# Kernel tuning notes

Measured on AMD Instinct MI355X. Metric: run time of the kernel, lower is better.

## Reference

```python
import jax, jax.numpy as jnp
import numpy as np

N_NODES = 50000
N_EDGES = 1600000
IN_CH = 512
HID_CH = 256


def _gcn_conv(x, edge_index, W, b):
    """PyG-style GCNConv: add self-loops, symmetric normalization, x@W then aggregate."""
    n = x.shape[0]
    loop = jnp.arange(n, dtype=edge_index.dtype)
    src = jnp.concatenate([edge_index[0], loop])  # [E+N]
    dst = jnp.concatenate([edge_index[1], loop])  # [E+N]
    deg = jax.ops.segment_sum(jnp.ones_like(dst, dtype=x.dtype), dst, num_segments=n)
    dinv = jnp.where(deg > 0, jax.lax.rsqrt(deg), 0.0)
    norm = dinv[src] * dinv[dst]  # [E+N]
    h = x @ W  # transform first (smaller feature dim for aggregation)
    msg = h[src] * norm[:, None]  # [E+N, F_out]
    out = jax.ops.segment_sum(msg, dst, num_segments=n)
    return out + b


def setup_inputs() -> dict:
    key = jax.random.key(0)
    ks = jax.random.split(key, 8)
    x = jax.random.normal(ks[0], (N_NODES, IN_CH), dtype=jnp.float32)
    edge_index = jax.random.randint(ks[1], (2, N_EDGES), 0, N_NODES, dtype=jnp.int32)
    W1 = jax.random.normal(ks[2], (IN_CH, HID_CH), dtype=jnp.float32) * (1.0 / np.sqrt(IN_CH))
    b1 = jnp.zeros((HID_CH,), dtype=jnp.float32)
    W2 = jax.random.normal(ks[3], (HID_CH, 32), dtype=jnp.float32) * (1.0 / np.sqrt(HID_CH))
    b2 = jnp.zeros((32,), dtype=jnp.float32)
    Wl = jax.random.normal(ks[4], (32, 2), dtype=jnp.float32) * (1.0 / np.sqrt(32))
    bl = jnp.zeros((2,), dtype=jnp.float32)
    return {"x": x, "edge_index": edge_index, "W1": W1, "b1": b1,
            "W2": W2, "b2": b2, "Wl": Wl, "bl": bl}


def reference(x, edge_index, W1, b1, W2, b2, Wl, bl):
    h = _gcn_conv(x, edge_index, W1, b1)
    h = jax.nn.relu(h)
    h = _gcn_conv(h, edge_index, W2, b2)
    # F.dropout(training=...) treated as identity (eval-mode reference)
    logits = h @ Wl + bl
    return jax.nn.log_softmax(logits, axis=1)
```

## Files before the change

### kernel.cpp

```cpp
#include <hip/hip_runtime.h>
#include <hip/hip_bf16.h>
#include <stdint.h>

#define NN 50000
#define NE 1600000
#define CIN 512
#define CH1 256
#define CH2 32

#define NBUCK 196
#define CAP 10240
#define CAP2 16384
#define ECH 4096
#define NCH 391

typedef __bf16 bf16_t;
typedef __attribute__((ext_vector_type(2))) __bf16 bf16x2;
typedef __attribute__((ext_vector_type(8))) __bf16 bf16x8;
typedef __attribute__((ext_vector_type(4))) float f32x4;

__device__ inline float blo(uint32_t v) { return __uint_as_float(v << 16); }
__device__ inline float bhi(uint32_t v) { return __uint_as_float(v & 0xffff0000u); }
__device__ inline uint32_t pk2(float a, float b) {
  bf16x2 p; p[0] = (__bf16)a; p[1] = (__bf16)b; return *(uint32_t*)&p;
}

__global__ __launch_bounds__(256) void k_hist(const int* __restrict__ dst,
                                              int* __restrict__ counts) {
  __shared__ int h[256];
  int blk = blockIdx.x, t = threadIdx.x;
  int e0 = blk * ECH;
  int ce = NE - e0; if (ce > ECH) ce = ECH;
  h[t] = 0;
  __syncthreads();
  for (int k = t; k < ce; k += 256) atomicAdd(&h[dst[e0 + k] >> 8], 1);
  __syncthreads();
  if (t < NBUCK) counts[blk * NBUCK + t] = h[t];
}

__global__ __launch_bounds__(512) void k_scanb(const int* __restrict__ counts,
                                               int* __restrict__ offs,
                                               int* __restrict__ bcnt) {
  __shared__ int l[512];
  int b = blockIdx.x, t = threadIdx.x;
  int v = (t < NCH) ? counts[t * NBUCK + b] : 0;
  int x = v;
  l[t] = x;
  __syncthreads();
  for (int off = 1; off < 512; off <<= 1) {
    int u = (t >= off) ? l[t - off] : 0;
    __syncthreads();
    x += u; l[t] = x;
    __syncthreads();
  }
  if (t < NCH) offs[t * NBUCK + b] = b * CAP + (x - v);
  if (t == 511) bcnt[b] = x;
}

__global__ __launch_bounds__(256) void k_bin(const int* __restrict__ src,
    const int* __restrict__ dst, const int* __restrict__ offs,
    uint32_t* __restrict__ binned) {
  __shared__ int h[256], lbase[256], lcnt[256], offsL[256];
  __shared__ uint32_t lstage[ECH];
  int blk = blockIdx.x, t = threadIdx.x;
  int e0 = blk * ECH;
  int ce = NE - e0; if (ce > ECH) ce = ECH;
  h[t] = 0; lcnt[t] = 0;
  if (t < NBUCK) offsL[t] = offs[blk * NBUCK + t];
  __syncthreads();
  for (int k = t; k < ce; k += 256) atomicAdd(&h[dst[e0 + k] >> 8], 1);
  __syncthreads();
  int v = h[t], x = v;
  lbase[t] = x;
  __syncthreads();
  for (int off = 1; off < 256; off <<= 1) {
    int u = (t >= off) ? lbase[t - off] : 0;
    __syncthreads();
    x += u; lbase[t] = x;
    __syncthreads();
  }
  lbase[t] = x - v;
  __syncthreads();
  for (int k = t; k < ce; k += 256) {
    int d = dst[e0 + k], s = src[e0 + k];
    int bkt = d >> 8;
    int p = lbase[bkt] + atomicAdd(&lcnt[bkt], 1);
    lstage[p] = ((uint32_t)bkt << 24) | ((uint32_t)(d & 255) << 16) | (uint32_t)s;
  }
  __syncthreads();
  for (int j = t; j < ce; j += 256) {
    uint32_t e = lstage[j];
    int bkt = e >> 24;
    binned[offsL[bkt] + (j - lbase[bkt])] = e & 0x00ffffffu;
  }
}

__global__ __launch_bounds__(256) void k_build(const uint32_t* __restrict__ binned,
    const int* __restrict__ bcnt, int* __restrict__ rowptr2, int* __restrict__ deg2,
    float* __restrict__ dinv, uint16_t* __restrict__ csrs) {
  __shared__ int hist[256], prow[256], lcnt[256];
  __shared__ int tot_s;
  __shared__ uint32_t c2[CAP2];
  int b = blockIdx.x, t = threadIdx.x;
  int count = bcnt[b];
  hist[t] = 0; lcnt[t] = 0;
  __syncthreads();
  const uint32_t* bb = binned + (size_t)b * CAP;
  for (int j = t; j < count; j += 256) atomicAdd(&hist[bb[j] >> 16], 1);
  __syncthreads();
  int node = b * 256 + t;
  int deg = hist[t];
  int pdeg = (node < NN) ? ((deg + 16) & ~15) : 0;
  int x = pdeg;
  prow[t] = x;
  __syncthreads();
  for (int off = 1; off < 256; off <<= 1) {
    int u = (t >= off) ? prow[t - off] : 0;
    __syncthreads();
    x += u; prow[t] = x;
    __syncthreads();
  }
  int start = x - pdeg;
  prow[t] = start;
  if (t == 255) tot_s = x;
  if (node < NN) {
    rowptr2[node] = b * CAP2 + start;
    deg2[node] = pdeg;
    dinv[node] = 1.0f / sqrtf((float)(deg + 1));
    c2[start + deg] = (uint32_t)node;
    for (int k = deg + 1; k < pdeg; ++k)
      c2[start + k] = (uint32_t)NN;
  }
  __syncthreads();
  for (int j = t; j < count; j += 256) {
    uint32_t e = bb[j];
    int dl = e >> 16;
    int p = prow[dl] + atomicAdd(&lcnt[dl], 1);
    c2[p] = e & 0xffffu;
  }
  __syncthreads();
  int tot = tot_s;
  uint16_t* co = csrs + (size_t)b * CAP2;
  for (int j = t; j < tot; j += 256) co[j] = (uint16_t)c2[j];
}

__global__ void k_prep_w(const float* __restrict__ W1, const float* __restrict__ W2,
                         bf16_t* __restrict__ w1t, bf16_t* __restrict__ w2t,
                         uint32_t* __restrict__ h1p_u32, uint32_t* __restrict__ h2b_u32) {
  int i = blockIdx.x * 256 + threadIdx.x;
  if (i < CIN * CH1) {
    int n = i >> 9, k = i & 511;
    w1t[i] = (__bf16)W1[k * CH1 + n];
  }
  if (i < CH1 * CH2) {
    int oc = i >> 8, k = i & 255;
    w2t[i] = (__bf16)W2[k * CH2 + oc];
  }
  if (blockIdx.x == 0) {
    int t = threadIdx.x;
    if (t < 128) {
      int p = t >> 4;
      h1p_u32[((size_t)p * (NN + 1) + NN) * 16 + (t & 15)] = 0;
    } else if (t < 144) {
      h2b_u32[(size_t)NN * 16 + (t - 128)] = 0;
    }
  }
}

#define BM 128
#define BN 128
#define BK 64

__global__ __launch_bounds__(256) void k_gemm1(const float* __restrict__ X,
                                               const bf16_t* __restrict__ BT,
                                               const float* __restrict__ dinv,
                                               bf16_t* __restrict__ h1p) {
  __shared__ __align__(16) bf16_t ldsA[2][BM * BK];
  __shared__ __align__(16) bf16_t ldsB[2][BN * BK];
  const int tid = threadIdx.x;
  const int lane = tid & 63;
  const int wid = tid >> 6;
  const int tm = blockIdx.x, tn = blockIdx.y;
  const int wm = wid >> 1, wn = wid & 1;

  f32x4 acc[4][4] = {};
  float4 ra[4], rb[4];

  auto loadA = [&](int kt) {
#pragma unroll
    for (int q = 0; q < 4; ++q) {
      int idx16 = q * 256 + tid;
      int r = idx16 >> 3, cw = idx16 & 7;
      int grow = tm * BM + r;
      grow = grow < NN ? grow : NN - 1;
      const float* ga = X + (size_t)grow * CIN + kt * BK + cw * 8;
      ra[q] = *(const float4*)ga;
      rb[q] = *(const float4*)(ga + 4);
    }
  };
  auto writeA = [&](int buf) {
#pragma unroll
    for (int q = 0; q < 4; ++q) {
      int idx16 = q * 256 + tid;
      int r = idx16 >> 3, cw = idx16 & 7;
      bf16x8 o;
      o[0] = (__bf16)ra[q].x; o[1] = (__bf16)ra[q].y;
      o[2] = (__bf16)ra[q].z; o[3] = (__bf16)ra[q].w;
      o[4] = (__bf16)rb[q].x; o[5] = (__bf16)rb[q].y;
      o[6] = (__bf16)rb[q].z; o[7] = (__bf16)rb[q].w;
      *(bf16x8*)&ldsA[buf][r * 64 + ((cw ^ (r & 7)) << 3)] = o;
    }
  };
  auto stageB = [&](int buf, int kt) {
#pragma unroll
    for (int t = 0; t < 4; ++t) {
      int o = t * 4096 + tid * 16;
      int r = o >> 7, cw = (o >> 4) & 7;
      int lc = cw ^ (r & 7);
      const bf16_t* gb = BT + (size_t)(tn * BN + r) * CIN + kt * BK + lc * 8;
      __builtin_amdgcn_global_load_lds(
          (const __attribute__((address_space(1))) void*)gb,
          (__attribute__((address_space(3))) void*)&ldsB[buf][(t * 4096 + wid * 1024) >> 1],
          16, 0, 0);
    }
  };

  loadA(0);
  stageB(0, 0);
  writeA(0);
  __syncthreads();
  int cur = 0;
  for (int kt = 0; kt < CIN / BK; ++kt) {
    if (kt + 1 < CIN / BK) { loadA(kt + 1); stageB(cur ^ 1, kt + 1); }
#pragma unroll
    for (int ks = 0; ks < 2; ++ks) {
      bf16x8 af[4], bfr[4];
#pragma unroll
      for (int m = 0; m < 4; ++m) {
        int row = wm * 64 + m * 16 + (lane & 15);
        int kc = ks * 4 + (lane >> 4);
        af[m] = *(const bf16x8*)&ldsA[cur][row * 64 + ((kc ^ (row & 7)) << 3)];
      }
#pragma unroll
      for (int n = 0; n < 4; ++n) {
        int col = wn * 64 + n * 16 + (lane & 15);
        int kc = ks * 4 + (lane >> 4);
        bfr[n] = *(const bf16x8*)&ldsB[cur][col * 64 + ((kc ^ (col & 7)) << 3)];
      }
#pragma unroll
      for (int m = 0; m < 4; ++m)
#pragma unroll
        for (int n = 0; n < 4; ++n)
          acc[m][n] = __builtin_amdgcn_mfma_f32_16x16x32_bf16(af[m], bfr[n], acc[m][n], 0, 0, 0);
    }
    if (kt + 1 < CIN / BK) writeA(cur ^ 1);
    __syncthreads();
    cur ^= 1;
  }

#pragma unroll
  for (int m = 0; m < 4; ++m) {
#pragma unroll
    for (int r = 0; r < 4; ++r) {
      int grow = tm * BM + wm * 64 + m * 16 + (lane >> 4) * 4 + r;
      if (grow < NN) {
        float dv = dinv[grow];
#pragma unroll
        for (int n = 0; n < 4; ++n) {
          int gcol = tn * BN + wn * 64 + n * 16 + (lane & 15);
          int plane = gcol >> 5, pc = gcol & 31;
          h1p[(size_t)plane * ((NN + 1) * 32) + (size_t)grow * 32 + pc] =
              (__bf16)(dv * acc[m][n][r]);
        }
      }
    }
  }
}

__global__ __launch_bounds__(256) void k_agg1(const uint32_t* __restrict__ h1p,
    const int* __restrict__ rowptr2, const int* __restrict__ deg2,
    const uint16_t* __restrict__ csrs, const float* __restrict__ dinv,
    const float* __restrict__ bias, uint32_t* __restrict__ hrp) {
  const int s = blockIdx.x & 7;
  const int lane = threadIdx.x & 63;
  const int wid = threadIdx.x >> 6;
  const int i = (blockIdx.x >> 3) * 16 + wid * 4 + (lane >> 4);
  const int cl = lane & 15;
  const uint32_t* __restrict__ P = h1p + (size_t)s * ((NN + 1) * 16);

  float a0 = 0.f, a1 = 0.f;
  const int base = rowptr2[i];
  const int pdeg = deg2[i];
  for (int b0 = 0; b0 < pdeg; b0 += 16) {
    int ld = (int)__builtin_nontemporal_load(&csrs[base + b0 + cl]);
#pragma unroll
    for (int e = 0; e < 16; ++e) {
      int src = __shfl(ld, (lane & 48) + e);
      uint32_t v = P[(src << 4) + cl];
      a0 += blo(v); a1 += bhi(v);
    }
  }
  float di = dinv[i];
  float2 bb = *(const float2*)&bias[s * 32 + cl * 2];
  uint32_t o = pk2(fmaxf(di * a0 + bb.x, 0.f), fmaxf(di * a1 + bb.y, 0.f));
  __builtin_nontemporal_store(o, &hrp[((size_t)s * NN + i) * 16 + cl]);
}

__global__ __launch_bounds__(256) void k_gemm2(const bf16_t* __restrict__ hrp,
    const bf16_t* __restrict__ w2t, const float* __restrict__ dinv,
    bf16_t* __restrict__ h2b) {
  const int lane = threadIdx.x & 63;
  const int gw = blockIdx.x * 4 + (threadIdx.x >> 6);
  const int r0 = gw * 16;
  if (r0 >= NN) return;
  int arow = r0 + (lane & 15);
  arow = arow < NN ? arow : NN - 1;
  const int kc = lane >> 4;
  f32x4 acc0 = {}, acc1 = {};
#pragma unroll
  for (int kb = 0; kb < 8; ++kb) {
    bf16x8 a  = *(const bf16x8*)&hrp[(size_t)kb * (NN * 32) + (size_t)arow * 32 + kc * 8];
    bf16x8 b0 = *(const bf16x8*)&w2t[(size_t)(lane & 15) * CH1 + kb * 32 + kc * 8];
    bf16x8 b1 = *(const bf16x8*)&w2t[(size_t)(16 + (lane & 15)) * CH1 + kb * 32 + kc * 8];
    acc0 = __builtin_amdgcn_mfma_f32_16x16x32_bf16(a, b0, acc0, 0, 0, 0);
    acc1 = __builtin_amdgcn_mfma_f32_16x16x32_bf16(a, b1, acc1, 0, 0, 0);
  }
#pragma unroll
  for (int r = 0; r < 4; ++r) {
    int rr = r0 + (lane >> 4) * 4 + r;
    if (rr < NN) {
      float dv = dinv[rr];
      h2b[(size_t)rr * CH2 + (lane & 15)]      = (__bf16)(dv * acc0[r]);
      h2b[(size_t)rr * CH2 + 16 + (lane & 15)] = (__bf16)(dv * acc1[r]);
    }
  }
}

__global__ __launch_bounds__(256) void k_agg2(const uint32_t* __restrict__ h2b,
    const int* __restrict__ rowptr2, const int* __restrict__ deg2,
    const uint16_t* __restrict__ csrs, const float* __restrict__ dinv,
    const float* __restrict__ b2, const float* __restrict__ Wl,
    const float* __restrict__ bl, float* __restrict__ out) {
  const int lane = threadIdx.x & 63;
  const int wid = threadIdx.x >> 6;
  const int i = blockIdx.x * 16 + wid * 4 + (lane >> 4);
  const int cl = lane & 15;

  float a0 = 0.f, a1 = 0.f;
  const int base = rowptr2[i];
  const int pdeg = deg2[i];
  for (int b0 = 0; b0 < pdeg; b0 += 16) {
    int ld = (int)__builtin_nontemporal_load(&csrs[base + b0 + cl]);
#pragma unroll
    for (int e = 0; e < 16; ++e) {
      int src = __shfl(ld, (lane & 48) + e);
      uint32_t v = h2b[(src << 4) + cl];
      a0 += blo(v); a1 += bhi(v);
    }
  }
  float di = dinv[i];
  float vv0 = di * a0 + b2[cl * 2];
  float vv1 = di * a1 + b2[cl * 2 + 1];
  const float2* Wl2 = (const float2*)Wl;
  float2 w0 = Wl2[cl * 2], w1 = Wl2[cl * 2 + 1];
  float lp0 = vv0 * w0.x + vv1 * w1.x;
  float lp1 = vv0 * w0.y + vv1 * w1.y;
#pragma unroll
  for (int off = 1; off < 16; off <<= 1) {
    lp0 += __shfl_xor(lp0, off);
    lp1 += __shfl_xor(lp1, off);
  }
  if (cl == 0) {
    float l0 = lp0 + bl[0], l1 = lp1 + bl[1];
    float m = fmaxf(l0, l1);
    float lse = m + logf(expf(l0 - m) + expf(l1 - m));
    float2 o; o.x = l0 - lse; o.y = l1 - lse;
    *(float2*)&out[i * 2] = o;
  }
}

extern "C" void kernel_launch(void* const* d_in, const int* in_sizes, int n_in,
                              void* d_out, int out_size, void* d_ws, size_t ws_size,
                              hipStream_t stream) {
  const float* x  = (const float*)d_in[0];
  const int*   ei = (const int*)d_in[1];
  const float* W1 = (const float*)d_in[2];
  const float* b1 = (const float*)d_in[3];
  const float* W2 = (const float*)d_in[4];
  const float* b2 = (const float*)d_in[5];
  const float* Wl = (const float*)d_in[6];
  const float* bl = (const float*)d_in[7];
  float* out = (float*)d_out;

  const int* src = ei;
  const int* dst = ei + NE;

  uint8_t* w = (uint8_t*)d_ws;
  auto alloc = [&](size_t bytes) { void* p = w; w += (bytes + 255) & ~(size_t)255; return p; };
  int*      counts = (int*)alloc((size_t)NCH * NBUCK * 4);
  int*      offs   = (int*)alloc((size_t)NCH * NBUCK * 4);
  int*      bcnt   = (int*)alloc((size_t)NBUCK * 4);
  uint32_t* binned = (uint32_t*)alloc((size_t)NBUCK * CAP * 4);
  uint16_t* csrs   = (uint16_t*)alloc((size_t)NBUCK * CAP2 * 2);
  int*      rowptr2= (int*)alloc((size_t)NN * 4);
  int*      deg2   = (int*)alloc((size_t)NN * 4);
  float*    dinv   = (float*)alloc((size_t)NN * 4);
  bf16_t*   w1t    = (bf16_t*)alloc((size_t)CIN * CH1 * 2);
  bf16_t*   w2t    = (bf16_t*)alloc((size_t)CH1 * CH2 * 2);
  bf16_t*   h1p    = (bf16_t*)alloc((size_t)(NN + 1) * CH1 * 2);
  bf16_t*   hrp    = (bf16_t*)alloc((size_t)NN * CH1 * 2);
  bf16_t*   h2b    = (bf16_t*)alloc((size_t)(NN + 1) * CH2 * 2);

  k_hist <<<NCH, 256, 0, stream>>>(dst, counts);
  k_scanb<<<NBUCK, 512, 0, stream>>>(counts, offs, bcnt);
  k_bin  <<<NCH, 256, 0, stream>>>(src, dst, offs, binned);
  k_build<<<NBUCK, 256, 0, stream>>>(binned, bcnt, rowptr2, deg2, dinv, csrs);

  k_prep_w<<<(CIN * CH1 + 255) / 256, 256, 0, stream>>>(W1, W2, w1t, w2t,
                                                        (uint32_t*)h1p, (uint32_t*)h2b);

  dim3 g1((NN + BM - 1) / BM, CH1 / BN);
  k_gemm1<<<g1, 256, 0, stream>>>(x, w1t, dinv, h1p);

  k_agg1<<<(NN / 16) * 8, 256, 0, stream>>>((const uint32_t*)h1p, rowptr2, deg2,
                                            csrs, dinv, b1, (uint32_t*)hrp);
  k_gemm2<<<(NN / 16 + 3) / 4, 256, 0, stream>>>(hrp, w2t, dinv, h2b);
  k_agg2<<<NN / 16, 256, 0, stream>>>((const uint32_t*)h2b, rowptr2, deg2, csrs,
                                      dinv, b2, Wl, bl, out);
}
```

Measured before the change: 231.9 us.

## Use 4 lanes per node with 16-byte gathers in aggregation kernels

Both aggregation kernels now map 4 lanes per destination node instead of 16. Each lane gathers 16 bytes (8 bf16 channels) per neighbour through a vectorized load, and neighbour indices are read as packed uint32 pairs and prefetched one chunk ahead. This cuts the number of memory instructions and shuffles per edge and raises the number of nodes per wave, which helps hide load latency. The cost is more registers per lane and a padded-degree assumption of multiples of 8, where reads past the end of a row rely on the padding layout.

```diff
diff --git a/kernel.cpp b/kernel.cpp
--- a/kernel.cpp
+++ b/kernel.cpp
@@ -18,6 +18,8 @@
 typedef __attribute__((ext_vector_type(2))) __bf16 bf16x2;
 typedef __attribute__((ext_vector_type(8))) __bf16 bf16x8;
 typedef __attribute__((ext_vector_type(4))) float f32x4;
+typedef __attribute__((ext_vector_type(2))) float f32x2;
+typedef __attribute__((ext_vector_type(4))) uint32_t u32x4;
 
 __device__ inline float blo(uint32_t v) { return __uint_as_float(v << 16); }
 __device__ inline float bhi(uint32_t v) { return __uint_as_float(v & 0xffff0000u); }
@@ -284,26 +286,46 @@
   const int s = blockIdx.x & 7;
   const int lane = threadIdx.x & 63;
   const int wid = threadIdx.x >> 6;
-  const int i = (blockIdx.x >> 3) * 16 + wid * 4 + (lane >> 4);
-  const int cl = lane & 15;
-  const uint32_t* __restrict__ P = h1p + (size_t)s * ((NN + 1) * 16);
-
-  float a0 = 0.f, a1 = 0.f;
+  int i = (blockIdx.x >> 3) * 64 + wid * 16 + (lane >> 2);
+  const bool valid = i < NN;
+  i = valid ? i : NN - 1;
+  const int cl = lane & 3;
+  const int grp = lane & 60;
+  const int cb = cl << 4;
+  const char* __restrict__ Pb = (const char*)(h1p + (size_t)s * ((NN + 1) * 16));
+
+  f32x2 a0 = {0.f, 0.f}, a1 = {0.f, 0.f}, a2 = {0.f, 0.f}, a3 = {0.f, 0.f};
   const int base = rowptr2[i];
   const int pdeg = deg2[i];
-  for (int b0 = 0; b0 < pdeg; b0 += 16) {
-    int ld = (int)__builtin_nontemporal_load(&csrs[base + b0 + cl]);
-#pragma unroll
-    for (int e = 0; e < 16; ++e) {
-      int src = __shfl(ld, (lane & 48) + e);
-      uint32_t v = P[(src << 4) + cl];
-      a0 += blo(v); a1 += bhi(v);
-    }
+  uint32_t ent = __builtin_nontemporal_load((const uint32_t*)&csrs[base + cl * 2]);
+  for (int b0 = 0; b0 < pdeg; b0 += 8) {
+    uint32_t ent_n = __builtin_nontemporal_load(
+        (const uint32_t*)&csrs[base + b0 + 8 + cl * 2]);
+    int s0 = (int)(ent & 0xffffu) << 6;
+    int s1 = (int)(ent >> 16) << 6;
+#pragma unroll
+    for (int e = 0; e < 8; ++e) {
+      int off = __shfl((e & 1) ? s1 : s0, grp + (e >> 1)) + cb;
+      u32x4 v = *(const u32x4*)(Pb + off);
+      f32x2 f0 = {blo(v.x), bhi(v.x)};
+      f32x2 f1 = {blo(v.y), bhi(v.y)};
+      f32x2 f2 = {blo(v.z), bhi(v.z)};
+      f32x2 f3 = {blo(v.w), bhi(v.w)};
+      a0 += f0; a1 += f1; a2 += f2; a3 += f3;
+    }
+    ent = ent_n;
   }
   float di = dinv[i];
-  float2 bb = *(const float2*)&bias[s * 32 + cl * 2];
-  uint32_t o = pk2(fmaxf(di * a0 + bb.x, 0.f), fmaxf(di * a1 + bb.y, 0.f));
-  __builtin_nontemporal_store(o, &hrp[((size_t)s * NN + i) * 16 + cl]);
+  float4 b0v = *(const float4*)&bias[s * 32 + cl * 8];
+  float4 b1v = *(const float4*)&bias[s * 32 + cl * 8 + 4];
+  u32x4 o;
+  o.x = pk2(fmaxf(di * a0.x + b0v.x, 0.f), fmaxf(di * a0.y + b0v.y, 0.f));
+  o.y = pk2(fmaxf(di * a1.x + b0v.z, 0.f), fmaxf(di * a1.y + b0v.w, 0.f));
+  o.z = pk2(fmaxf(di * a2.x + b1v.x, 0.f), fmaxf(di * a2.y + b1v.y, 0.f));
+  o.w = pk2(fmaxf(di * a3.x + b1v.z, 0.f), fmaxf(di * a3.y + b1v.w, 0.f));
+  if (valid)
+    __builtin_nontemporal_store(o,
+        (u32x4*)&hrp[((size_t)s * NN + i) * 16 + cl * 4]);
 }
 
 __global__ __launch_bounds__(256) void k_gemm2(const bf16_t* __restrict__ hrp,
@@ -343,34 +365,52 @@
     const float* __restrict__ bl, float* __restrict__ out) {
   const int lane = threadIdx.x & 63;
   const int wid = threadIdx.x >> 6;
-  const int i = blockIdx.x * 16 + wid * 4 + (lane >> 4);
-  const int cl = lane & 15;
-
-  float a0 = 0.f, a1 = 0.f;
+  int i = blockIdx.x * 64 + wid * 16 + (lane >> 2);
+  const bool valid = i < NN;
+  i = valid ? i : NN - 1;
+  const int cl = lane & 3;
+  const int grp = lane & 60;
+  const int cb = cl << 4;
+  const char* __restrict__ Pb = (const char*)h2b;
+
+  f32x2 a0 = {0.f, 0.f}, a1 = {0.f, 0.f}, a2 = {0.f, 0.f}, a3 = {0.f, 0.f};
   const int base = rowptr2[i];
   const int pdeg = deg2[i];
-  for (int b0 = 0; b0 < pdeg; b0 += 16) {
-    int ld = (int)__builtin_nontemporal_load(&csrs[base + b0 + cl]);
-#pragma unroll
-    for (int e = 0; e < 16; ++e) {
-      int src = __shfl(ld, (lane & 48) + e);
-      uint32_t v = h2b[(src << 4) + cl];
-      a0 += blo(v); a1 += bhi(v);
-    }
+  uint32_t ent = __builtin_nontemporal_load((const uint32_t*)&csrs[base + cl * 2]);
+  for (int b0 = 0; b0 < pdeg; b0 += 8) {
+    uint32_t ent_n = __builtin_nontemporal_load(
+        (const uint32_t*)&csrs[base + b0 + 8 + cl * 2]);
+    int s0 = (int)(ent & 0xffffu) << 6;
+    int s1 = (int)(ent >> 16) << 6;
+#pragma unroll
+    for (int e = 0; e < 8; ++e) {
+      int off = __shfl((e & 1) ? s1 : s0, grp + (e >> 1)) + cb;
+      u32x4 v = *(const u32x4*)(Pb + off);
+      f32x2 f0 = {blo(v.x), bhi(v.x)};
+      f32x2 f1 = {blo(v.y), bhi(v.y)};
+      f32x2 f2 = {blo(v.z), bhi(v.z)};
+      f32x2 f3 = {blo(v.w), bhi(v.w)};
+      a0 += f0; a1 += f1; a2 += f2; a3 += f3;
+    }
+    ent = ent_n;
   }
   float di = dinv[i];
-  float vv0 = di * a0 + b2[cl * 2];
-  float vv1 = di * a1 + b2[cl * 2 + 1];
+  float vv[8];
+  vv[0] = di * a0.x + b2[cl * 8 + 0]; vv[1] = di * a0.y + b2[cl * 8 + 1];
+  vv[2] = di * a1.x + b2[cl * 8 + 2]; vv[3] = di * a1.y + b2[cl * 8 + 3];
+  vv[4] = di * a2.x + b2[cl * 8 + 4]; vv[5] = di * a2.y + b2[cl * 8 + 5];
+  vv[6] = di * a3.x + b2[cl * 8 + 6]; vv[7] = di * a3.y + b2[cl * 8 + 7];
+  float lp0 = 0.f, lp1 = 0.f;
   const float2* Wl2 = (const float2*)Wl;
-  float2 w0 = Wl2[cl * 2], w1 = Wl2[cl * 2 + 1];
-  float lp0 = vv0 * w0.x + vv1 * w1.x;
-  float lp1 = vv0 * w0.y + vv1 * w1.y;
-#pragma unroll
-  for (int off = 1; off < 16; off <<= 1) {
-    lp0 += __shfl_xor(lp0, off);
-    lp1 += __shfl_xor(lp1, off);
-  }
-  if (cl == 0) {
+#pragma unroll
+  for (int k = 0; k < 8; ++k) {
+    float2 wl = Wl2[cl * 8 + k];
+    lp0 += vv[k] * wl.x;
+    lp1 += vv[k] * wl.y;
+  }
+  lp0 += __shfl_xor(lp0, 1); lp0 += __shfl_xor(lp0, 2);
+  lp1 += __shfl_xor(lp1, 1); lp1 += __shfl_xor(lp1, 2);
+  if (valid && cl == 0) {
     float l0 = lp0 + bl[0], l1 = lp1 + bl[1];
     float m = fmaxf(l0, l1);
     float lse = m + logf(expf(l0 - m) + expf(l1 - m));
@@ -422,9 +462,10 @@
   dim3 g1((NN + BM - 1) / BM, CH1 / BN);
   k_gemm1<<<g1, 256, 0, stream>>>(x, w1t, dinv, h1p);
 
-  k_agg1<<<(NN / 16) * 8, 256, 0, stream>>>((const uint32_t*)h1p, rowptr2, deg2,
-                                            csrs, dinv, b1, (uint32_t*)hrp);
+  int nb = (NN + 63) / 64;
+  k_agg1<<<nb * 8, 256, 0, stream>>>((const uint32_t*)h1p, rowptr2, deg2,
+                                     csrs, dinv, b1, (uint32_t*)hrp);
   k_gemm2<<<(NN / 16 + 3) / 4, 256, 0, stream>>>(hrp, w2t, dinv, h2b);
-  k_agg2<<<NN / 16, 256, 0, stream>>>((const uint32_t*)h2b, rowptr2, deg2, csrs,
-                                      dinv, b2, Wl, bl, out);
-}
+  k_agg2<<<nb, 256, 0, stream>>>((const uint32_t*)h2b, rowptr2, deg2, csrs,
+                                 dinv, b2, Wl, bl, out);
+}
```

After: 235.8 us. About the same (+1.7%).
